# Performance work log

Hardware: AMD Instinct MI355X
Metric: run time of the kernel (lower is better)

## Reference

```python
import jax, jax.numpy as jnp
import numpy as np

N_HEADS = 64
HEAD_DIM = 128
TOPK = 2048
CHUNK = 256          # indexer_max_chunk_size analogue (Q-block chunking)
FP8_MAX = 448.0      # e4m3 max


def _hadamard_matrix(n):
    H = np.array([[1.0]], dtype=np.float32)
    while H.shape[0] < n:
        H = np.block([[H, H], [H, -H]])
    return jnp.asarray(H, dtype=jnp.float32)

_HM = _hadamard_matrix(HEAD_DIM)


def rotate_activation(x):
    # hadamard_transform(x, scale=hidden^-0.5)
    return (x @ _HM) * (HEAD_DIM ** -0.5)


def _fp8_quant(x):
    # per-last-dim-block (block == head_dim == 128) dynamic fp8 e4m3 quantization
    amax = jnp.max(jnp.abs(x), axis=-1, keepdims=True)
    scale = jnp.maximum(amax, 1e-4) / FP8_MAX
    xq = (x / scale).astype(jnp.float8_e4m3fn).astype(jnp.float32)
    # straight-through: value == quantized, gradient == identity
    xq = x / scale + jax.lax.stop_gradient(xq - x / scale)
    return xq, scale


def setup_inputs() -> dict:
    key = jax.random.key(0)
    k1, k2, k3 = jax.random.split(key, 3)
    T = 4096
    q = jax.random.normal(k1, (T, N_HEADS, HEAD_DIM), dtype=jnp.float32)
    k = jax.random.normal(k2, (T, HEAD_DIM), dtype=jnp.float32)
    weights = jax.random.uniform(k3, (T, N_HEADS), dtype=jnp.float32)
    seq_lens = jnp.full((2,), 2048, dtype=jnp.int32)  # 2 packed sequences
    return {"q": q, "k": k, "weights": weights, "seq_lens": seq_lens}


def reference(q, k, weights, seq_lens):
    T, H, D = q.shape

    # 1) Hadamard rotation of q and k activations
    qr = rotate_activation(q)           # [T, H, D]
    kr = rotate_activation(k)           # [T, D]

    # 2) fp8 quantization with per-(token,head) / per-token scales
    qf, q_scale = _fp8_quant(qr)        # qf [T,H,D], q_scale [T,H,1]
    kf, k_scale = _fp8_quant(kr)        # kf [T,D],   k_scale [T,1]

    # 3) _scale: fold q scales + softmax scale into routing weights
    softmax_scale = D ** -0.5
    w = weights * q_scale[..., 0] * softmax_scale   # [T, H]

    # 4) causal KV bounds per packed token (compute_cu_seqlen_kv_bounds_nocache)
    offs = jnp.concatenate([jnp.zeros(1, jnp.int32), jnp.cumsum(seq_lens).astype(jnp.int32)])
    batch_ids = jnp.repeat(jnp.arange(seq_lens.shape[0], dtype=jnp.int32), seq_lens,
                           total_repeat_length=T)
    cu_ks = offs[batch_ids]                          # start of own sequence
    pos = jnp.arange(T, dtype=jnp.int32)
    cu_ke = pos + 1                                  # causal end (exclusive)

    # 5) chunked indexer logits: I[t,s] = k_scale[s] * sum_h w[t,h]*relu(qf[t,h]Âkf[s])
    n_chunks = T // CHUNK
    q_chunks = qf.reshape(n_chunks, CHUNK, H, D)
    w_chunks = w.reshape(n_chunks, CHUNK, H)

    def body(carry, inp):
        qc, wc = inp                                  # [C,H,D], [C,H]
        sc = jnp.einsum('chd,sd->chs', qc, kf)        # fp8-style GEMM
        lc = jnp.einsum('ch,chs->cs', wc, jax.nn.relu(sc))
        return carry, lc

    _, lg = jax.lax.scan(body, None, (q_chunks, w_chunks))
    logits = lg.reshape(T, T) * k_scale[:, 0][None, :]

    # 6) causal mask from bounds, then top-k KV selection
    mask = (pos[None, :] >= cu_ks[:, None]) & (pos[None, :] < cu_ke[:, None])
    masked = jnp.where(mask, logits, -jnp.inf)
    _, topk_idx = jax.lax.top_k(masked, TOPK)
    return masked, topk_idx.astype(jnp.int32)
```

## Files before the change

### kernel.cpp

```cpp
#include <hip/hip_runtime.h>
#include <stdint.h>

#define HEADS 64
#define HD 128
#define TOPK_N 2048
#define BT 32
#define BS 256
#define XCAP 256

typedef float f32x4 __attribute__((ext_vector_type(4)));
typedef long  lx2  __attribute__((ext_vector_type(2)));

static constexpr float RSQRT_D = 0.08838834764831845f;

__device__ inline unsigned short pk_fp8(float a, float b) {
    int r = __builtin_amdgcn_cvt_pk_fp8_f32(a, b, 0, false);
    return (unsigned short)(r & 0xffff);
}

__device__ inline int perm_src_lane(int m) {
    return ((m & 0x0C) << 2) | ((m & 0x30) >> 2) | (m & 3);
}

__device__ inline void fwht128(float& a, float& b, int lane) {
    float na = a + b, nb = a - b;
    a = na; b = nb;
#pragma unroll
    for (int m = 1; m < 64; m <<= 1) {
        float pa = __shfl_xor(a, m, 64);
        float pb = __shfl_xor(b, m, 64);
        bool hi = (lane & m) != 0;
        a = hi ? (pa - a) : (a + pa);
        b = hi ? (pb - b) : (b + pb);
    }
}

__global__ __launch_bounds__(256)
void k_rotquant(const float* __restrict__ kin, uint8_t* __restrict__ kf,
                float* __restrict__ k_scale, int T) {
    int wave = (int)((blockIdx.x * blockDim.x + threadIdx.x) >> 6);
    int lane = threadIdx.x & 63;
    if (wave >= T) return;
    const float2 v = ((const float2*)(kin + (size_t)wave * HD))[lane];
    float a = v.x, b = v.y;
    fwht128(a, b, lane);
    a *= RSQRT_D; b *= RSQRT_D;
    float amax = fmaxf(fabsf(a), fabsf(b));
#pragma unroll
    for (int m = 1; m < 64; m <<= 1) amax = fmaxf(amax, __shfl_xor(amax, m, 64));
    float scale = fmaxf(amax, 1e-4f) / 448.0f;
    int pk = (int)pk_fp8(a / scale, b / scale);
    int g = __shfl(pk, perm_src_lane(lane), 64);
    *(unsigned short*)(kf + (size_t)wave * HD + lane * 2) = (unsigned short)g;
    if (lane == 0) k_scale[wave] = scale;
}

__global__ __launch_bounds__(256)
void q_rotquant(const float* __restrict__ q, const float* __restrict__ weights,
                uint8_t* __restrict__ qh, float* __restrict__ wprime, int T) {
    int row = (int)((blockIdx.x * blockDim.x + threadIdx.x) >> 6);
    int lane = threadIdx.x & 63;
    if (row >= T * HEADS) return;
    int t = row >> 6, h = row & 63;
    const float2 v = ((const float2*)(q + (size_t)row * HD))[lane];
    float a = v.x, b = v.y;
    fwht128(a, b, lane);
    a *= RSQRT_D; b *= RSQRT_D;
    float amax = fmaxf(fabsf(a), fabsf(b));
#pragma unroll
    for (int m = 1; m < 64; m <<= 1) amax = fmaxf(amax, __shfl_xor(amax, m, 64));
    float scale = fmaxf(amax, 1e-4f) / 448.0f;
    int tb = t >> 5, r = t & 31;
    int pk = (int)pk_fp8(a / scale, b / scale);
    int g = __shfl(pk, perm_src_lane(lane), 64);
    size_t dst = ((((size_t)tb * HEADS + h) << 5) + r) * HD + lane * 2;
    *(unsigned short*)(qh + dst) = (unsigned short)g;
    if (lane == 0) wprime[row] = (weights[row] * scale) * RSQRT_D;
}

__global__ void bounds_kernel(const int* __restrict__ seq_lens, int B,
                              int* __restrict__ cu_ks, int T) {
    __shared__ int offs[130];
    if (threadIdx.x == 0) {
        int acc = 0; offs[0] = 0;
        for (int b = 0; b < B && b < 128; b++) { acc += seq_lens[b]; offs[b + 1] = acc; }
    }
    __syncthreads();
    int t = blockIdx.x * blockDim.x + threadIdx.x;
    if (t < T) {
        int b = 0;
        while (b < B - 1 && offs[b + 1] <= t) b++;
        cu_ks[t] = offs[b];
    }
}

__global__ __launch_bounds__(128)
void queue_kernel(const int* __restrict__ cu_ks, int* __restrict__ tiles,
                  int* __restrict__ cnt, int T) {
    int nb = T / BT;
    int tid = threadIdx.x;
    int x = tid >> 4, i = tid & 15;
    int y = i * 8 + x;
    int c = 0, sbmin = 0;
    if (y < nb) {
        int t0 = y * BT;
        sbmin = cu_ks[t0] / BS;
        c = (t0 + BT - 1) / BS - sbmin + 1;
    }
    unsigned int incl = (unsigned int)c;
#pragma unroll
    for (int o = 1; o < 16; o <<= 1) {
        unsigned int v = __shfl_up(incl, o, 16);
        if (i >= o) incl += v;
    }
    unsigned int excl = incl - (unsigned int)c;
    if (y < nb)
        for (int k = 0; k < c; k++)
            tiles[x * XCAP + excl + k] = (y << 8) | (sbmin + k);
    if (i == 15) cnt[x] = (int)incl;
}

__global__ __launch_bounds__(256)
void gemm_kernel(const uint8_t* __restrict__ qh, const uint8_t* __restrict__ kf,
                 const float* __restrict__ wprime, const float* __restrict__ k_scale,
                 const int* __restrict__ tiles, const int* __restrict__ cnt,
                 float* __restrict__ outF, int T) {
    int x = blockIdx.x & 7, j = blockIdx.x >> 3;
    if (j >= cnt[x]) return;
    int tile = tiles[x * XCAP + j];
    int y = tile >> 8, sb = tile & 255;
    int t0 = y * BT, s0 = sb * BS;

    int tid = threadIdx.x, lane = tid & 63, w = tid >> 6;
    int wr = w >> 1, wc = w & 1;
    int lrow = lane & 15, lk = lane >> 4;

    __shared__ float wlds[HEADS * BT];
    {
        const float* src = wprime + (size_t)t0 * HEADS;
        for (int i = tid; i < HEADS * BT; i += 256) {
            wlds[(i & 63) * BT + (i >> 6)] = src[i];
        }
    }
    __syncthreads();

    const f32x4 zero4 = {0.f, 0.f, 0.f, 0.f};
    const size_t HS = BT * HD;

    int rt = t0 + wr * 16;
    int cs = s0 + wc * 128;
    int tmax = t0 + BT - 1;
    int ntv = ((tmax - cs) >> 4) + 1;
    if (ntv > 8) ntv = 8;
    if (ntv <= 0) return;

    long bfrag[8][4];
#pragma unroll
    for (int nt = 0; nt < 8; nt++) {
        const uint8_t* bp = kf + (size_t)(cs + nt * 16 + lrow) * HD + lk * 32;
        lx2 b01 = *(const lx2*)(bp);
        lx2 b23 = *(const lx2*)(bp + 16);
        bfrag[nt][0] = b01.x; bfrag[nt][1] = b01.y;
        bfrag[nt][2] = b23.x; bfrag[nt][3] = b23.y;
    }

    f32x4 acc[8];
#pragma unroll
    for (int nt = 0; nt < 8; nt++) acc[nt] = zero4;

    const uint8_t* abase = qh + ((((size_t)(t0 >> 5) * HEADS) << 5)
                                 + (wr * 16 + lrow)) * HD + lk * 32;
    const float* wvbase = wlds + (size_t)(wr * 16 + lk * 4);

#define LOADA(j, hh) { const uint8_t* qp = abase + (size_t)(hh) * HS; \
        pa[j] = *(const lx2*)(qp); pb[j] = *(const lx2*)(qp + 16); }
#define COMP(j, hh) { \
        f32x4 wv = *(const f32x4*)(wvbase + ((hh) << 5)); \
        f32x4 sc[8]; \
        _Pragma("unroll") \
        for (int nt = 0; nt < 8; nt++) \
            sc[nt] = __builtin_amdgcn_mfma_f32_16x16x32_fp8_fp8(pa[j].x, bfrag[nt][0], zero4, 0, 0, 0); \
        _Pragma("unroll") \
        for (int nt = 0; nt < 8; nt++) \
            sc[nt] = __builtin_amdgcn_mfma_f32_16x16x32_fp8_fp8(pa[j].y, bfrag[nt][1], sc[nt], 0, 0, 0); \
        _Pragma("unroll") \
        for (int nt = 0; nt < 8; nt++) \
            sc[nt] = __builtin_amdgcn_mfma_f32_16x16x32_fp8_fp8(pb[j].x, bfrag[nt][2], sc[nt], 0, 0, 0); \
        _Pragma("unroll") \
        for (int nt = 0; nt < 8; nt++) \
            sc[nt] = __builtin_amdgcn_mfma_f32_16x16x32_fp8_fp8(pb[j].y, bfrag[nt][3], sc[nt], 0, 0, 0); \
        _Pragma("unroll") \
        for (int nt = 0; nt < 8; nt++) \
            acc[nt] += wv * __builtin_elementwise_max(sc[nt], zero4); \
    }

    lx2 pa[4], pb[4];
#pragma unroll
    for (int j = 0; j < 4; j++) LOADA(j, j);

    for (int h = 0; h < HEADS; h += 4) {
#pragma unroll
        for (int j = 0; j < 4; j++) {
            COMP(j, h + j);
            LOADA(j, (h + 4 + j) & 63);
        }
    }
#undef LOADA
#undef COMP

#pragma unroll
    for (int nt = 0; nt < 8; nt++) if (nt < ntv) {
        int s = cs + nt * 16 + lrow;
        float ksc = k_scale[s];
#pragma unroll
        for (int r = 0; r < 4; r++) {
            int t = rt + lk * 4 + r;
            outF[(size_t)t * T + s] = acc[nt][r] * ksc;
        }
    }
}

__global__ __launch_bounds__(512)
void sort_kernel(const float* __restrict__ outF, const int* __restrict__ cu_ks,
                 int* __restrict__ outI, int T) {
    int t = blockIdx.x;
    int tid = threadIdx.x, lane = tid & 63, wv = tid >> 6;
    int ks = cu_ks[t];
    int n = t - ks + 1;

    __shared__ unsigned long long pkA[2048];
    __shared__ unsigned long long pkB[2048];
    __shared__ unsigned int hist[2048];
    __shared__ unsigned int sred[16];
    __shared__ unsigned int wpart[8];
    __shared__ unsigned int sdmin;
    __shared__ unsigned long long sinv;

    const float* row = outF + (size_t)t * T + ks;
    unsigned int dmin = 0xFFFFFFFFu, dmax = 0u;
    for (int i = tid; i < n; i += 512) {
        unsigned int u = __float_as_uint(row[i]);
        unsigned int asc = u ^ ((u >> 31) ? 0xFFFFFFFFu : 0x80000000u);
        unsigned int dk = ~asc;
        pkA[i] = ((unsigned long long)dk << 32) | (unsigned int)i;
        dmin = min(dmin, dk); dmax = max(dmax, dk);
    }
#pragma unroll
    for (int o = 1; o < 64; o <<= 1) {
        dmin = min(dmin, (unsigned int)__shfl_xor((int)dmin, o, 64));
        dmax = max(dmax, (unsigned int)__shfl_xor((int)dmax, o, 64));
    }
    if (lane == 0) { sred[wv] = dmin; sred[8 + wv] = dmax; }
    for (int i = tid; i < 2048; i += 512) hist[i] = 0;
    __syncthreads();
    if (tid == 0) {
        unsigned int mn = sred[0], mx = sred[8];
#pragma unroll
        for (int j = 1; j < 8; j++) { mn = min(mn, sred[j]); mx = max(mx, sred[8 + j]); }
        unsigned int range = mx - mn;
        sdmin = mn;
        sinv = range ? ((2047ULL << 32) / range) : 0ULL;
    }
    __syncthreads();
    const unsigned int mn = sdmin;
    const unsigned long long inv = sinv;

    for (int i = tid; i < n; i += 512) {
        unsigned int dk = (unsigned int)(pkA[i] >> 32);
        unsigned int b = min((unsigned int)(((unsigned long long)(dk - mn) * inv) >> 32), 2047u);
        atomicAdd(&hist[b], 1u);
    }
    __syncthreads();

    unsigned int h0 = hist[tid * 4 + 0], h1 = hist[tid * 4 + 1];
    unsigned int h2 = hist[tid * 4 + 2], h3 = hist[tid * 4 + 3];
    unsigned int s4 = h0 + h1 + h2 + h3;
    unsigned int incl = s4;
#pragma unroll
    for (int o = 1; o < 64; o <<= 1) {
        unsigned int v = __shfl_up(incl, o, 64);
        if (lane >= o) incl += v;
    }
    if (lane == 63) wpart[wv] = incl;
    __syncthreads();
    unsigned int wbase = 0;
#pragma unroll
    for (int j = 0; j < 8; j++) wbase += (j < wv) ? wpart[j] : 0;
    unsigned int excl = wbase + incl - s4;
    hist[tid * 4 + 0] = excl;
    hist[tid * 4 + 1] = excl + h0;
    hist[tid * 4 + 2] = excl + h0 + h1;
    hist[tid * 4 + 3] = excl + h0 + h1 + h2;
    __syncthreads();

    for (int i = tid; i < n; i += 512) {
        unsigned long long pk = pkA[i];
        unsigned int dk = (unsigned int)(pk >> 32);
        unsigned int b = min((unsigned int)(((unsigned long long)(dk - mn) * inv) >> 32), 2047u);
        unsigned int pos = atomicAdd(&hist[b], 1u);
        pkB[pos] = pk;
    }
    __syncthreads();

    for (int b = tid; b < 2048; b += 512) {
        int e = (int)hist[b];
        int s = (b == 0) ? 0 : (int)hist[b - 1];
        for (int i = s + 1; i < e; i++) {
            unsigned long long key = pkB[i];
            int j = i - 1;
            while (j >= s && pkB[j] > key) { pkB[j + 1] = pkB[j]; j--; }
            pkB[j + 1] = key;
        }
    }
    __syncthreads();

    for (int j = tid; j < TOPK_N; j += 512) {
        int v;
        if (j < n) v = ks + (int)(pkB[j] & 0xFFFFu);
        else { int f = j - n; v = (f < ks) ? f : (t + 1) + (f - ks); }
        outI[(size_t)t * TOPK_N + j] = v;
    }
}

extern "C" void kernel_launch(void* const* d_in, const int* in_sizes, int n_in,
                              void* d_out, int out_size, void* d_ws, size_t ws_size,
                              hipStream_t stream) {
    const float* q       = (const float*)d_in[0];
    const float* k       = (const float*)d_in[1];
    const float* weights = (const float*)d_in[2];
    const int* seq_lens  = (const int*)d_in[3];

    int T = in_sizes[1] / HD;
    int B = in_sizes[3];

    uint8_t* ws = (uint8_t*)d_ws;
    size_t off = 0;
    uint8_t* kf    = ws;                    off += (size_t)T * HD;
    float* k_scale = (float*)(ws + off);    off += (size_t)T * 4;
    float* wprime  = (float*)(ws + off);    off += (size_t)T * HEADS * 4;
    uint8_t* qh    = ws + off;              off += (size_t)T * HEADS * HD;
    int* cu_ks     = (int*)(ws + off);      off += (size_t)T * 4;
    int* tiles     = (int*)(ws + off);      off += (size_t)8 * XCAP * 4;
    int* cnt       = (int*)(ws + off);      off += 64;

    float* outF = (float*)d_out;
    int* outI   = (int*)d_out + (size_t)T * T;

    k_rotquant<<<(T + 3) / 4, 256, 0, stream>>>(k, kf, k_scale, T);
    q_rotquant<<<(T * HEADS + 3) / 4, 256, 0, stream>>>(q, weights, qh, wprime, T);
    bounds_kernel<<<(T + 255) / 256, 256, 0, stream>>>(seq_lens, B, cu_ks, T);
    queue_kernel<<<1, 128, 0, stream>>>(cu_ks, tiles, cnt, T);

    gemm_kernel<<<2048, 256, 0, stream>>>(qh, kf, wprime, k_scale, tiles, cnt, outF, T);

    sort_kernel<<<T, 512, 0, stream>>>(outF, cu_ks, outI, T);
}
```

Before: 192.4 us.

## Rework row top-k sort to use float bucketing, drop staging buffer, halve block size

The per-row sort kernel no longer stages packed keys in a 16KB shared array. It computes the float min and max directly, then re-reads the row from global memory for the histogram and scatter passes. Buckets come from a float scale instead of 64-bit integer multiplies, and the block shrinks to 256 threads with 8 histogram bins per thread in the scan. This cuts shared memory per block to raise occupancy, at the cost of extra global/L2 reads of each row.

```diff
diff --git a/kernel.cpp b/kernel.cpp
--- a/kernel.cpp
+++ b/kernel.cpp
@@ -220,7 +220,7 @@
     }
 }
 
-__global__ __launch_bounds__(512)
+__global__ __launch_bounds__(256)
 void sort_kernel(const float* __restrict__ outF, const int* __restrict__ cu_ks,
                  int* __restrict__ outI, int T) {
     int t = blockIdx.x;
@@ -228,54 +228,49 @@
     int ks = cu_ks[t];
     int n = t - ks + 1;
 
-    __shared__ unsigned long long pkA[2048];
     __shared__ unsigned long long pkB[2048];
     __shared__ unsigned int hist[2048];
-    __shared__ unsigned int sred[16];
-    __shared__ unsigned int wpart[8];
-    __shared__ unsigned int sdmin;
-    __shared__ unsigned long long sinv;
+    __shared__ float fred[8];
+    __shared__ unsigned int wpart[4];
+    __shared__ float svmax, sscale;
 
     const float* row = outF + (size_t)t * T + ks;
-    unsigned int dmin = 0xFFFFFFFFu, dmax = 0u;
-    for (int i = tid; i < n; i += 512) {
-        unsigned int u = __float_as_uint(row[i]);
-        unsigned int asc = u ^ ((u >> 31) ? 0xFFFFFFFFu : 0x80000000u);
-        unsigned int dk = ~asc;
-        pkA[i] = ((unsigned long long)dk << 32) | (unsigned int)i;
-        dmin = min(dmin, dk); dmax = max(dmax, dk);
+
+    float vmin = 3.4e38f, vmax = -3.4e38f;
+    for (int i = tid; i < n; i += 256) {
+        float v = row[i];
+        vmin = fminf(vmin, v); vmax = fmaxf(vmax, v);
     }
 #pragma unroll
     for (int o = 1; o < 64; o <<= 1) {
-        dmin = min(dmin, (unsigned int)__shfl_xor((int)dmin, o, 64));
-        dmax = max(dmax, (unsigned int)__shfl_xor((int)dmax, o, 64));
-    }
-    if (lane == 0) { sred[wv] = dmin; sred[8 + wv] = dmax; }
-    for (int i = tid; i < 2048; i += 512) hist[i] = 0;
+        vmin = fminf(vmin, __shfl_xor(vmin, o, 64));
+        vmax = fmaxf(vmax, __shfl_xor(vmax, o, 64));
+    }
+    if (lane == 0) { fred[wv] = vmin; fred[4 + wv] = vmax; }
+    for (int i = tid; i < 2048; i += 256) hist[i] = 0;
     __syncthreads();
     if (tid == 0) {
-        unsigned int mn = sred[0], mx = sred[8];
-#pragma unroll
-        for (int j = 1; j < 8; j++) { mn = min(mn, sred[j]); mx = max(mx, sred[8 + j]); }
-        unsigned int range = mx - mn;
-        sdmin = mn;
-        sinv = range ? ((2047ULL << 32) / range) : 0ULL;
-    }
-    __syncthreads();
-    const unsigned int mn = sdmin;
-    const unsigned long long inv = sinv;
-
-    for (int i = tid; i < n; i += 512) {
-        unsigned int dk = (unsigned int)(pkA[i] >> 32);
-        unsigned int b = min((unsigned int)(((unsigned long long)(dk - mn) * inv) >> 32), 2047u);
+        float mn = fred[0], mx = fred[4];
+#pragma unroll
+        for (int j = 1; j < 4; j++) { mn = fminf(mn, fred[j]); mx = fmaxf(mx, fred[4 + j]); }
+        float range = mx - mn;
+        svmax = mx;
+        sscale = (range > 0.f) ? (2047.0f / range) : 0.f;
+    }
+    __syncthreads();
+    const float vmx = svmax, scl = sscale;
+
+    for (int i = tid; i < n; i += 256) {
+        unsigned int b = (unsigned int)((vmx - row[i]) * scl);
+        if (b > 2047u) b = 2047u;
         atomicAdd(&hist[b], 1u);
     }
     __syncthreads();
 
-    unsigned int h0 = hist[tid * 4 + 0], h1 = hist[tid * 4 + 1];
-    unsigned int h2 = hist[tid * 4 + 2], h3 = hist[tid * 4 + 3];
-    unsigned int s4 = h0 + h1 + h2 + h3;
-    unsigned int incl = s4;
+    unsigned int hloc[8], s8 = 0;
+#pragma unroll
+    for (int k = 0; k < 8; k++) { hloc[k] = hist[tid * 8 + k]; s8 += hloc[k]; }
+    unsigned int incl = s8;
 #pragma unroll
     for (int o = 1; o < 64; o <<= 1) {
         unsigned int v = __shfl_up(incl, o, 64);
@@ -283,26 +278,27 @@
     }
     if (lane == 63) wpart[wv] = incl;
     __syncthreads();
-    unsigned int wbase = 0;
-#pragma unroll
-    for (int j = 0; j < 8; j++) wbase += (j < wv) ? wpart[j] : 0;
-    unsigned int excl = wbase + incl - s4;
-    hist[tid * 4 + 0] = excl;
-    hist[tid * 4 + 1] = excl + h0;
-    hist[tid * 4 + 2] = excl + h0 + h1;
-    hist[tid * 4 + 3] = excl + h0 + h1 + h2;
-    __syncthreads();
-
-    for (int i = tid; i < n; i += 512) {
-        unsigned long long pk = pkA[i];
-        unsigned int dk = (unsigned int)(pk >> 32);
-        unsigned int b = min((unsigned int)(((unsigned long long)(dk - mn) * inv) >> 32), 2047u);
+    unsigned int base = 0;
+#pragma unroll
+    for (int j = 0; j < 4; j++) base += (j < wv) ? wpart[j] : 0;
+    unsigned int run = base + incl - s8;
+#pragma unroll
+    for (int k = 0; k < 8; k++) { hist[tid * 8 + k] = run; run += hloc[k]; }
+    __syncthreads();
+
+    for (int i = tid; i < n; i += 256) {
+        float v = row[i];
+        unsigned int u = __float_as_uint(v);
+        unsigned int asc = u ^ ((u >> 31) ? 0xFFFFFFFFu : 0x80000000u);
+        unsigned int dk = ~asc;
+        unsigned int b = (unsigned int)((vmx - v) * scl);
+        if (b > 2047u) b = 2047u;
         unsigned int pos = atomicAdd(&hist[b], 1u);
-        pkB[pos] = pk;
-    }
-    __syncthreads();
-
-    for (int b = tid; b < 2048; b += 512) {
+        pkB[pos] = ((unsigned long long)dk << 32) | (unsigned int)i;
+    }
+    __syncthreads();
+
+    for (int b = tid; b < 2048; b += 256) {
         int e = (int)hist[b];
         int s = (b == 0) ? 0 : (int)hist[b - 1];
         for (int i = s + 1; i < e; i++) {
@@ -314,7 +310,7 @@
     }
     __syncthreads();
 
-    for (int j = tid; j < TOPK_N; j += 512) {
+    for (int j = tid; j < TOPK_N; j += 256) {
         int v;
         if (j < n) v = ks + (int)(pkB[j] & 0xFFFFu);
         else { int f = j - n; v = (f < ks) ? f : (t + 1) + (f - ks); }
@@ -353,5 +349,5 @@
 
     gemm_kernel<<<2048, 256, 0, stream>>>(qh, kf, wprime, k_scale, tiles, cnt, outF, T);
 
-    sort_kernel<<<T, 512, 0, stream>>>(outF, cu_ks, outI, T);
-}
+    sort_kernel<<<T, 256, 0, stream>>>(outF, cu_ks, outI, T);
+}
```

Result: no change. 190.2 us (-1.2%).
